# Kernel optimization log

Measured on AMD Instinct MI355X. Metric: run time of the kernel, lower is better.

## Reference

```python
import jax, jax.numpy as jnp
import numpy as np

N_NODES = 20000
N_EDGES = 200000
D_MODEL = 128
N_HEADS = 8
N_LAYERS = 2  # num_gnn - 1 concat layers


def setup_inputs() -> dict:
    key = jax.random.key(0)
    ks = jax.random.split(key, 12)
    s = 0.05  # keep activations well-scaled across residual layers
    hd = D_MODEL // N_HEADS  # 16
    return {
        "x": jax.random.normal(ks[0], (N_NODES, D_MODEL), jnp.float32),
        "src": jax.random.randint(ks[1], (N_EDGES,), 0, N_NODES),
        "dst": jax.random.randint(ks[2], (N_EDGES,), 0, N_NODES),
        "Ws": jax.random.normal(ks[3], (N_LAYERS, D_MODEL, D_MODEL), jnp.float32) * s,
        "als": jax.random.normal(ks[4], (N_LAYERS, N_HEADS, hd), jnp.float32) * s,
        "ars": jax.random.normal(ks[5], (N_LAYERS, N_HEADS, hd), jnp.float32) * s,
        "bs": jax.random.normal(ks[6], (N_LAYERS, D_MODEL), jnp.float32) * s,
        "W_last": jax.random.normal(ks[7], (D_MODEL, N_HEADS * D_MODEL), jnp.float32) * s,
        "al_last": jax.random.normal(ks[8], (N_HEADS, D_MODEL), jnp.float32) * s,
        "ar_last": jax.random.normal(ks[9], (N_HEADS, D_MODEL), jnp.float32) * s,
        "b_last": jax.random.normal(ks[10], (N_HEADS * D_MODEL,), jnp.float32) * s,
    }


def gat_conv(h, src, dst, W, al, ar, b, num_nodes):
    """DGL GATConv (eval mode, dropout off): returns (N, H, D) head outputs."""
    H, D = al.shape
    feat = (h @ W).reshape(num_nodes, H, D)          # (N,H,D)
    el = jnp.sum(feat * al[None], axis=-1)           # (N,H) attn on src side
    er = jnp.sum(feat * ar[None], axis=-1)           # (N,H) attn on dst side
    e = jax.nn.leaky_relu(el[src] + er[dst], 0.2)    # (E,H)
    # edge softmax over incoming edges of each dst node, per head
    m = jax.ops.segment_max(e, dst, num_segments=num_nodes)  # (N,H)
    p = jnp.exp(e - m[dst])                          # (E,H)
    z = jax.ops.segment_sum(p, dst, num_segments=num_nodes)  # (N,H)
    a = p / z[dst]                                   # (E,H)
    msg = feat[src] * a[..., None]                   # (E,H,D) weighted messages
    rst = jax.ops.segment_sum(msg, dst, num_segments=num_nodes)  # (N,H,D)
    return rst + b.reshape(1, H, D)


def reference(x, src, dst, Ws, als, ars, bs, W_last, al_last, ar_last, b_last):
    N = x.shape[0]
    h = x
    for i in range(N_LAYERS):
        temp = gat_conv(h, src, dst, Ws[i], als[i], ars[i], bs[i], N)  # (N,H,hd)
        h = h + jax.nn.elu(temp.reshape(N, -1))       # concat heads, ELU, residual
    temp = gat_conv(h, src, dst, W_last, al_last, ar_last, b_last, N)  # (N,H,D)
    h = h + jnp.mean(temp, axis=1)                    # mean over heads, residual
    return h
```

## Files before the change

kernel.cpp:

```cpp
#include <hip/hip_runtime.h>
#include <math.h>

#define N_NODES 20000
#define N_EDGES 200000
#define DM 128
#define NH 8

typedef __attribute__((ext_vector_type(8))) short bf16x8;
typedef __attribute__((ext_vector_type(4))) float f32x4;

__device__ __forceinline__ unsigned short f2b(float f) {
  unsigned int u = __float_as_uint(f);
  unsigned int r = (u + 0x7FFFu + ((u >> 16) & 1u)) >> 16;
  return (unsigned short)r;
}
__device__ __forceinline__ float b2f(unsigned short s) {
  return __uint_as_float(((unsigned int)s) << 16);
}

__global__ __launch_bounds__(256) void degzero(int* __restrict__ deg) {
  int i = blockIdx.x * 256 + threadIdx.x;
  if (i < N_NODES) deg[i] = 0;
}

__global__ __launch_bounds__(256) void prep_all(
    const float* __restrict__ x, float* __restrict__ h, unsigned short* __restrict__ hb,
    const int* __restrict__ dstE, int* __restrict__ deg, int* __restrict__ rank,
    const float* __restrict__ Ws, unsigned short* __restrict__ wsz,
    const float* __restrict__ W_last, unsigned short* __restrict__ wpsz,
    const float* __restrict__ al_last, const float* __restrict__ ar_last,
    const float* __restrict__ b_last, unsigned short* __restrict__ wlrsz,
    float* __restrict__ mb) {
  int i = blockIdx.x * 256 + threadIdx.x;
  if (i < (N_NODES * DM) / 4) {
    float4 v = ((const float4*)x)[i];
    ((float4*)h)[i] = v;
    ((ushort4*)hb)[i] = make_ushort4(f2b(v.x), f2b(v.y), f2b(v.z), f2b(v.w));
  }
  if (i < N_EDGES) rank[i] = atomicAdd(&deg[dstE[i]], 1);
  if (i < 2 * 16384) {
    int layer = i >> 14;
    int r = i & 16383;
    int j = r & 7, l = (r >> 3) & 63, f = (r >> 9) & 7, ks = r >> 12;
    int k = ks * 32 + ((l >> 4) << 3) + j;
    int n = f * 16 + (l & 15);
    wsz[i] = f2b(Ws[(size_t)layer * 16384 + k * 128 + n]);
  }
  if (i < 131072) {
    int j = i & 7, l = (i >> 3) & 63, f = (i >> 9) & 7, ks = i >> 12;
    int k = ks * 32 + ((l >> 4) << 3) + j;
    int n = f * 16 + (l & 15);
    int h_ = k >> 7, ko = k & 127;
    wpsz[i] = f2b(W_last[(size_t)ko * 1024 + h_ * 128 + n] * 0.125f);
  }
  if (i < 2048) {
    int j = i & 7, l = (i >> 3) & 63, ks = i >> 9;
    int k = ks * 32 + ((l >> 4) << 3) + j;
    int n = l & 15;
    int hh = n & 7;
    const float* av = (n < 8) ? (al_last + hh * 128) : (ar_last + hh * 128);
    float s = 0.f;
    for (int d = 0; d < 128; ++d) s += W_last[(size_t)k * 1024 + hh * 128 + d] * av[d];
    wlrsz[i] = f2b(s);
  }
  if (i < 128) {
    float s = 0.f;
#pragma unroll
    for (int hh = 0; hh < 8; ++hh) s += b_last[hh * 128 + i];
    mb[i] = s * 0.125f;
  }
}

__global__ void scan_deg(const int* __restrict__ deg, int* __restrict__ off) {
  __shared__ int part[1024];
  const int tid = threadIdx.x;
  const int CHUNK = (N_NODES + 1023) / 1024;
  int base = tid * CHUNK;
  int s = 0;
  for (int i = 0; i < CHUNK; ++i) {
    int idx = base + i;
    if (idx < N_NODES) s += deg[idx];
  }
  part[tid] = s;
  __syncthreads();
  for (int ofs = 1; ofs < 1024; ofs <<= 1) {
    int v = (tid >= ofs) ? part[tid - ofs] : 0;
    __syncthreads();
    part[tid] += v;
    __syncthreads();
  }
  int run = (tid > 0) ? part[tid - 1] : 0;
  for (int i = 0; i < CHUNK; ++i) {
    int idx = base + i;
    if (idx < N_NODES) {
      off[idx] = run;
      run += deg[idx];
    }
  }
  if (tid == 0) off[N_NODES] = part[1023];
}

template <int K, bool LAST>
__device__ __forceinline__ void dev_gemm(int tile, const unsigned short* __restrict__ A,
                                         const unsigned short* __restrict__ Bsz,
                                         const float* __restrict__ hres,
                                         const float* __restrict__ mbv,
                                         unsigned short* __restrict__ Cb,
                                         float* __restrict__ Cf,
                                         const float* __restrict__ al,
                                         const float* __restrict__ ar,
                                         float* __restrict__ elr, int lane, int wid) {
  const int wrow = wid & 1, wc = wid >> 1;
  const int r0 = tile * 32;
  const int arow = r0 + wrow * 16 + (lane & 15);
  const int kg = lane >> 4;

  f32x4 acc[4];
#pragma unroll
  for (int fi = 0; fi < 4; ++fi) acc[fi] = {0.f, 0.f, 0.f, 0.f};

  const bf16x8* Ap = (const bf16x8*)(A + (size_t)arow * K + kg * 8);
#pragma unroll 4
  for (int ks = 0; ks < K / 32; ++ks) {
    bf16x8 a = Ap[ks * 4];
#pragma unroll
    for (int fi = 0; fi < 4; ++fi) {
      int f = wc * 4 + fi;
      bf16x8 b = *(const bf16x8*)(Bsz + (((size_t)(ks * 8 + f) * 64 + lane) << 3));
      acc[fi] = __builtin_amdgcn_mfma_f32_16x16x32_bf16(a, b, acc[fi], 0, 0, 0);
    }
  }

  const int rbase = r0 + wrow * 16 + (lane >> 4) * 4;
#pragma unroll
  for (int fi = 0; fi < 4; ++fi) {
    int col = wc * 64 + fi * 16 + (lane & 15);
#pragma unroll
    for (int r = 0; r < 4; ++r) {
      int row = rbase + r;
      float v = acc[fi][r];
      if (LAST)
        Cf[(size_t)row * DM + col] = v + hres[(size_t)row * DM + col] + mbv[col];
      else
        Cb[(size_t)row * DM + col] = f2b(v);
    }
  }

  if (!LAST) {
#pragma unroll
    for (int fi = 0; fi < 4; ++fi) {
      int hh = wc * 4 + fi;
      float alv = al[hh * 16 + (lane & 15)];
      float arv = ar[hh * 16 + (lane & 15)];
#pragma unroll
      for (int r = 0; r < 4; ++r) {
        float pl = acc[fi][r] * alv;
        float pr = acc[fi][r] * arv;
#pragma unroll
        for (int msk = 1; msk < 16; msk <<= 1) {
          pl += __shfl_xor(pl, msk, 64);
          pr += __shfl_xor(pr, msk, 64);
        }
        if ((lane & 15) == 0) {
          int row = rbase + r;
          elr[row * 16 + hh] = pl;
          elr[row * 16 + 8 + hh] = pr;
        }
      }
    }
  }
}

__global__ __launch_bounds__(256) void gemm0_scatter(
    const unsigned short* __restrict__ A, const unsigned short* __restrict__ Bsz,
    unsigned short* __restrict__ Cb, const float* __restrict__ al,
    const float* __restrict__ ar, float* __restrict__ elr, const int* __restrict__ srcE,
    const int* __restrict__ dstE, const int* __restrict__ rank,
    const int* __restrict__ off, int* __restrict__ csr_src) {
  const int bid = blockIdx.x;
  if (bid < N_NODES / 32) {
    dev_gemm<DM, false>(bid, A, Bsz, nullptr, nullptr, Cb, nullptr, al, ar, elr,
                        threadIdx.x & 63, threadIdx.x >> 6);
  } else {
    int e = (bid - N_NODES / 32) * 256 + threadIdx.x;
    if (e < N_EDGES) {
      csr_src[off[dstE[e]] + rank[e]] = srcE[e];
    }
  }
}

template <int K, bool LAST>
__global__ __launch_bounds__(256) void gemm_mfma(
    const unsigned short* __restrict__ A, const unsigned short* __restrict__ Bsz,
    const float* __restrict__ hres, const float* __restrict__ mbv,
    unsigned short* __restrict__ Cb, float* __restrict__ Cf,
    const float* __restrict__ al, const float* __restrict__ ar, float* __restrict__ elr) {
  dev_gemm<K, LAST>(blockIdx.x, A, Bsz, hres, mbv, Cb, Cf, al, ar, elr, threadIdx.x & 63,
                    threadIdx.x >> 6);
}

template <bool ELR>
__global__ __launch_bounds__(256) void fused_small(
    const int* __restrict__ off, const int* __restrict__ csr_src,
    const unsigned short* __restrict__ feat, const float* __restrict__ elr,
    const float* __restrict__ bias, float* __restrict__ h, unsigned short* __restrict__ hb,
    const unsigned short* __restrict__ wlrsz, float* __restrict__ elr_out) {
  __shared__ float a_lds[4][64];
  __shared__ int s_lds[4][8];
  __shared__ float zi_lds[4][8];
  __shared__ __align__(16) unsigned short nh_lds[4][128];
  const int wid = threadIdx.x >> 6;
  const int t = blockIdx.x * 4 + wid;
  const int lane = threadIdx.x & 63;
  const int e_loc = lane >> 3, hh = lane & 7;
  const int hg = lane >> 3;
  const int beg = off[t], end = off[t + 1];
  const float ert = elr[t * 16 + 8 + hh];

  int e = beg + e_loc;
  bool val = e < end;
  int s = val ? csr_src[e] : 0;
  float xl = val ? elr[s * 16 + hh] : 0.f;

  float z = 0.f, acc0 = 0.f, acc1 = 0.f;
  for (int base = beg; base < end; base += 8) {
    float ex = 0.f;
    if (val) {
      float xv = xl + ert;
      xv = xv > 0.f ? xv : 0.2f * xv;
      ex = __expf(xv);
    }
    a_lds[wid][lane] = ex;
    if (hh == 0) s_lds[wid][e_loc] = s;
    __builtin_amdgcn_wave_barrier();
    asm volatile("s_waitcnt lgkmcnt(0)" ::: "memory");
    z += ex;
    int en = base + 8 + e_loc;
    bool valn = en < end;
    int sn = valn ? csr_src[en] : 0;
    float xln = valn ? elr[sn * 16 + hh] : 0.f;
    int n = min(8, end - base);
    for (int e2 = 0; e2 < n; ++e2) {
      int s2 = s_lds[wid][e2];
      float a = a_lds[wid][e2 * 8 + hg];
      unsigned int hv = *(const unsigned int*)&feat[(size_t)s2 * 128 + 2 * lane];
      acc0 += a * b2f((unsigned short)(hv & 0xffffu));
      acc1 += a * b2f((unsigned short)(hv >> 16));
    }
    __builtin_amdgcn_wave_barrier();
    s = sn;
    xl = xln;
    val = valn;
  }
  z += __shfl_xor(z, 8, 64);
  z += __shfl_xor(z, 16, 64);
  z += __shfl_xor(z, 32, 64);
  if (e_loc == 0) zi_lds[wid][hh] = (z > 0.f) ? 1.f / z : 0.f;
  __builtin_amdgcn_wave_barrier();
  asm volatile("s_waitcnt lgkmcnt(0)" ::: "memory");
  float zi = zi_lds[wid][hg];

  float2 bv = *(const float2*)&bias[2 * lane];
  float v0 = acc0 * zi + bv.x;
  float v1 = acc1 * zi + bv.y;
  v0 = v0 > 0.f ? v0 : expm1f(v0);
  v1 = v1 > 0.f ? v1 : expm1f(v1);
  size_t idx = (size_t)t * 128 + 2 * lane;
  float2 hv = *(const float2*)&h[idx];
  float nh0 = hv.x + v0;
  float nh1 = hv.y + v1;
  *(float2*)&h[idx] = make_float2(nh0, nh1);
  unsigned short b0 = f2b(nh0), b1 = f2b(nh1);
  *(ushort2*)&hb[idx] = make_ushort2(b0, b1);

  if (ELR) {
    *(ushort2*)&nh_lds[wid][2 * lane] = make_ushort2(b0, b1);
    __builtin_amdgcn_wave_barrier();
    asm volatile("s_waitcnt lgkmcnt(0)" ::: "memory");
    const int kg = lane >> 4;
    f32x4 acc = {0.f, 0.f, 0.f, 0.f};
#pragma unroll
    for (int ks = 0; ks < 4; ++ks) {
      bf16x8 a = *(const bf16x8*)&nh_lds[wid][ks * 32 + kg * 8];
      bf16x8 b = *(const bf16x8*)(wlrsz + (((size_t)ks * 64 + lane) << 3));
      acc = __builtin_amdgcn_mfma_f32_16x16x32_bf16(a, b, acc, 0, 0, 0);
    }
    if (lane < 16) elr_out[t * 16 + lane] = acc[0];
  }
}

__global__ __launch_bounds__(256) void fused_last(
    const int* __restrict__ off, const int* __restrict__ csr_src,
    const unsigned short* __restrict__ hb, const float* __restrict__ elr,
    unsigned short* __restrict__ g) {
  __shared__ float a_lds[4][64];
  __shared__ int s_lds[4][8];
  __shared__ float zi_lds[4][8];
  const int wid = threadIdx.x >> 6;
  const int t = blockIdx.x * 4 + wid;
  const int lane = threadIdx.x & 63;
  const int e_loc = lane >> 3, hh = lane & 7;
  const int beg = off[t], end = off[t + 1];
  const float ert = elr[t * 16 + 8 + hh];

  int e = beg + e_loc;
  bool val = e < end;
  int s = val ? csr_src[e] : 0;
  float xl = val ? elr[s * 16 + hh] : 0.f;

  float z = 0.f;
  float accA[8], accB[8];
#pragma unroll
  for (int k = 0; k < 8; ++k) accA[k] = accB[k] = 0.f;

  for (int base = beg; base < end; base += 8) {
    float ex = 0.f;
    if (val) {
      float xv = xl + ert;
      xv = xv > 0.f ? xv : 0.2f * xv;
      ex = __expf(xv);
    }
    a_lds[wid][lane] = ex;
    if (hh == 0) s_lds[wid][e_loc] = s;
    __builtin_amdgcn_wave_barrier();
    asm volatile("s_waitcnt lgkmcnt(0)" ::: "memory");
    z += ex;
    int en = base + 8 + e_loc;
    bool valn = en < end;
    int sn = valn ? csr_src[en] : 0;
    float xln = valn ? elr[sn * 16 + hh] : 0.f;
    int n = min(8, end - base);
    for (int e2 = 0; e2 < n; ++e2) {
      int s2 = s_lds[wid][e2];
      float4 pa = *(const float4*)&a_lds[wid][e2 * 8];
      float4 pb = *(const float4*)&a_lds[wid][e2 * 8 + 4];
      unsigned int hv = *(const unsigned int*)&hb[(size_t)s2 * 128 + 2 * lane];
      float h0 = b2f((unsigned short)(hv & 0xffffu));
      float h1 = b2f((unsigned short)(hv >> 16));
      accA[0] += pa.x * h0; accB[0] += pa.x * h1;
      accA[1] += pa.y * h0; accB[1] += pa.y * h1;
      accA[2] += pa.z * h0; accB[2] += pa.z * h1;
      accA[3] += pa.w * h0; accB[3] += pa.w * h1;
      accA[4] += pb.x * h0; accB[4] += pb.x * h1;
      accA[5] += pb.y * h0; accB[5] += pb.y * h1;
      accA[6] += pb.z * h0; accB[6] += pb.z * h1;
      accA[7] += pb.w * h0; accB[7] += pb.w * h1;
    }
    __builtin_amdgcn_wave_barrier();
    s = sn;
    xl = xln;
    val = valn;
  }
  z += __shfl_xor(z, 8, 64);
  z += __shfl_xor(z, 16, 64);
  z += __shfl_xor(z, 32, 64);
  if (e_loc == 0) zi_lds[wid][hh] = (z > 0.f) ? 1.f / z : 0.f;
  __builtin_amdgcn_wave_barrier();
  asm volatile("s_waitcnt lgkmcnt(0)" ::: "memory");
  float4 zia = *(const float4*)&zi_lds[wid][0];
  float4 zib = *(const float4*)&zi_lds[wid][4];
  float ziv[8] = {zia.x, zia.y, zia.z, zia.w, zib.x, zib.y, zib.z, zib.w};
#pragma unroll
  for (int h2 = 0; h2 < 8; ++h2) {
    *(ushort2*)&g[(size_t)t * 1024 + h2 * 128 + 2 * lane] =
        make_ushort2(f2b(accA[h2] * ziv[h2]), f2b(accB[h2] * ziv[h2]));
  }
}

extern "C" void kernel_launch(void* const* d_in, const int* in_sizes, int n_in,
                              void* d_out, int out_size, void* d_ws, size_t ws_size,
                              hipStream_t stream) {
  const float* x = (const float*)d_in[0];
  const int* src = (const int*)d_in[1];
  const int* dst = (const int*)d_in[2];
  const float* Ws = (const float*)d_in[3];
  const float* als = (const float*)d_in[4];
  const float* ars = (const float*)d_in[5];
  const float* bs = (const float*)d_in[6];
  const float* W_last = (const float*)d_in[7];
  const float* al_last = (const float*)d_in[8];
  const float* ar_last = (const float*)d_in[9];
  const float* b_last = (const float*)d_in[10];
  float* out = (float*)d_out;

  float* h = (float*)d_ws;
  float* elr = h + 2560000;
  float* elr2 = elr + 320000;
  float* mb = elr2 + 320000;
  unsigned short* hb = (unsigned short*)(mb + 128);
  unsigned short* feat = hb + 2560000;
  unsigned short* g = feat + 2560000;
  unsigned short* wsz = g + 20480000;
  unsigned short* wpsz = wsz + 32768;
  unsigned short* wlrsz = wpsz + 131072;
  int* deg = (int*)(wlrsz + 2048);
  int* off = deg + N_NODES;
  int* rank = off + N_NODES + 1;
  int* csr_src = rank + N_EDGES;

  const int GB = N_NODES / 32;
  const int FB = N_NODES / 4;
  const int EB = (N_EDGES + 255) / 256;

  degzero<<<(N_NODES + 255) / 256, 256, 0, stream>>>(deg);
  prep_all<<<(N_NODES * DM / 4 + 255) / 256, 256, 0, stream>>>(
      x, h, hb, dst, deg, rank, Ws, wsz, W_last, wpsz, al_last, ar_last, b_last, wlrsz, mb);
  scan_deg<<<1, 1024, 0, stream>>>(deg, off);
  gemm0_scatter<<<GB + EB, 256, 0, stream>>>(hb, wsz, feat, als, ars, elr, src, dst, rank,
                                             off, csr_src);
  fused_small<false><<<FB, 256, 0, stream>>>(off, csr_src, feat, elr, bs, h, hb, nullptr,
                                             nullptr);
  gemm_mfma<DM, false><<<GB, 256, 0, stream>>>(hb, wsz + 16384, nullptr, nullptr, feat,
                                               nullptr, als + 128, ars + 128, elr);
  fused_small<true><<<FB, 256, 0, stream>>>(off, csr_src, feat, elr, bs + 128, h, hb,
                                            wlrsz, elr2);
  fused_last<<<FB, 256, 0, stream>>>(off, csr_src, hb, elr2, g);
  gemm_mfma<NH * DM, true><<<GB, 256, 0, stream>>>(g, wpsz, h, mb, nullptr, out, nullptr,
                                                   nullptr, nullptr);
}
```

Measured before the change: 184.5 us.

## Fuse last-layer aggregation with output projection GEMM through LDS

Merges the last layer's edge aggregation kernel and the final K=1024 projection GEMM into one kernel. Each 1024-thread block aggregates 16 nodes into an LDS tile, then sixteen waves run MFMA over split K halves and reduce through LDS before adding the residual and bias. This removes the 40MB bf16 intermediate g write and read plus one launch. In exchange, per-block occupancy drops with large LDS use and 1024-thread blocks, and each block reloads the projection weights.

```diff
diff --git a/kernel.cpp b/kernel.cpp
--- a/kernel.cpp
+++ b/kernel.cpp
@@ -100,13 +100,10 @@
   if (tid == 0) off[N_NODES] = part[1023];
 }
 
-template <int K, bool LAST>
+template <int K>
 __device__ __forceinline__ void dev_gemm(int tile, const unsigned short* __restrict__ A,
                                          const unsigned short* __restrict__ Bsz,
-                                         const float* __restrict__ hres,
-                                         const float* __restrict__ mbv,
                                          unsigned short* __restrict__ Cb,
-                                         float* __restrict__ Cf,
                                          const float* __restrict__ al,
                                          const float* __restrict__ ar,
                                          float* __restrict__ elr, int lane, int wid) {
@@ -137,35 +134,28 @@
     int col = wc * 64 + fi * 16 + (lane & 15);
 #pragma unroll
     for (int r = 0; r < 4; ++r) {
-      int row = rbase + r;
-      float v = acc[fi][r];
-      if (LAST)
-        Cf[(size_t)row * DM + col] = v + hres[(size_t)row * DM + col] + mbv[col];
-      else
-        Cb[(size_t)row * DM + col] = f2b(v);
-    }
-  }
-
-  if (!LAST) {
-#pragma unroll
-    for (int fi = 0; fi < 4; ++fi) {
-      int hh = wc * 4 + fi;
-      float alv = al[hh * 16 + (lane & 15)];
-      float arv = ar[hh * 16 + (lane & 15)];
-#pragma unroll
-      for (int r = 0; r < 4; ++r) {
-        float pl = acc[fi][r] * alv;
-        float pr = acc[fi][r] * arv;
-#pragma unroll
-        for (int msk = 1; msk < 16; msk <<= 1) {
-          pl += __shfl_xor(pl, msk, 64);
-          pr += __shfl_xor(pr, msk, 64);
-        }
-        if ((lane & 15) == 0) {
-          int row = rbase + r;
-          elr[row * 16 + hh] = pl;
-          elr[row * 16 + 8 + hh] = pr;
-        }
+      Cb[(size_t)(rbase + r) * DM + col] = f2b(acc[fi][r]);
+    }
+  }
+
+#pragma unroll
+  for (int fi = 0; fi < 4; ++fi) {
+    int hh = wc * 4 + fi;
+    float alv = al[hh * 16 + (lane & 15)];
+    float arv = ar[hh * 16 + (lane & 15)];
+#pragma unroll
+    for (int r = 0; r < 4; ++r) {
+      float pl = acc[fi][r] * alv;
+      float pr = acc[fi][r] * arv;
+#pragma unroll
+      for (int msk = 1; msk < 16; msk <<= 1) {
+        pl += __shfl_xor(pl, msk, 64);
+        pr += __shfl_xor(pr, msk, 64);
+      }
+      if ((lane & 15) == 0) {
+        int row = rbase + r;
+        elr[row * 16 + hh] = pl;
+        elr[row * 16 + 8 + hh] = pr;
       }
     }
   }
@@ -179,8 +169,7 @@
     const int* __restrict__ off, int* __restrict__ csr_src) {
   const int bid = blockIdx.x;
   if (bid < N_NODES / 32) {
-    dev_gemm<DM, false>(bid, A, Bsz, nullptr, nullptr, Cb, nullptr, al, ar, elr,
-                        threadIdx.x & 63, threadIdx.x >> 6);
+    dev_gemm<DM>(bid, A, Bsz, Cb, al, ar, elr, threadIdx.x & 63, threadIdx.x >> 6);
   } else {
     int e = (bid - N_NODES / 32) * 256 + threadIdx.x;
     if (e < N_EDGES) {
@@ -189,14 +178,11 @@
   }
 }
 
-template <int K, bool LAST>
 __global__ __launch_bounds__(256) void gemm_mfma(
     const unsigned short* __restrict__ A, const unsigned short* __restrict__ Bsz,
-    const float* __restrict__ hres, const float* __restrict__ mbv,
-    unsigned short* __restrict__ Cb, float* __restrict__ Cf,
-    const float* __restrict__ al, const float* __restrict__ ar, float* __restrict__ elr) {
-  dev_gemm<K, LAST>(blockIdx.x, A, Bsz, hres, mbv, Cb, Cf, al, ar, elr, threadIdx.x & 63,
-                    threadIdx.x >> 6);
+    unsigned short* __restrict__ Cb, const float* __restrict__ al,
+    const float* __restrict__ ar, float* __restrict__ elr) {
+  dev_gemm<DM>(blockIdx.x, A, Bsz, Cb, al, ar, elr, threadIdx.x & 63, threadIdx.x >> 6);
 }
 
 template <bool ELR>
@@ -289,81 +275,118 @@
   }
 }
 
-__global__ __launch_bounds__(256) void fused_last(
+#define GT_STRIDE 1032
+__global__ __launch_bounds__(1024) void agg_gemm16(
     const int* __restrict__ off, const int* __restrict__ csr_src,
     const unsigned short* __restrict__ hb, const float* __restrict__ elr,
-    unsigned short* __restrict__ g) {
-  __shared__ float a_lds[4][64];
-  __shared__ int s_lds[4][8];
-  __shared__ float zi_lds[4][8];
+    const unsigned short* __restrict__ wpsz, const float* __restrict__ hres,
+    const float* __restrict__ mb, float* __restrict__ out) {
+  __shared__ __align__(16) unsigned short gt[16][GT_STRIDE];
+  __shared__ float red[8][64][4];
+  __shared__ float a_lds[16][64];
+  __shared__ int s_lds[16][8];
+  __shared__ float zi_lds[16][8];
   const int wid = threadIdx.x >> 6;
-  const int t = blockIdx.x * 4 + wid;
   const int lane = threadIdx.x & 63;
+  const int t0 = blockIdx.x * 16;
+  const int t = t0 + wid;
   const int e_loc = lane >> 3, hh = lane & 7;
-  const int beg = off[t], end = off[t + 1];
-  const float ert = elr[t * 16 + 8 + hh];
-
-  int e = beg + e_loc;
-  bool val = e < end;
-  int s = val ? csr_src[e] : 0;
-  float xl = val ? elr[s * 16 + hh] : 0.f;
-
-  float z = 0.f;
-  float accA[8], accB[8];
-#pragma unroll
-  for (int k = 0; k < 8; ++k) accA[k] = accB[k] = 0.f;
-
-  for (int base = beg; base < end; base += 8) {
-    float ex = 0.f;
-    if (val) {
-      float xv = xl + ert;
-      xv = xv > 0.f ? xv : 0.2f * xv;
-      ex = __expf(xv);
-    }
-    a_lds[wid][lane] = ex;
-    if (hh == 0) s_lds[wid][e_loc] = s;
+
+  {
+    const int beg = off[t], end = off[t + 1];
+    const float ert = elr[t * 16 + 8 + hh];
+    int e = beg + e_loc;
+    bool val = e < end;
+    int s = val ? csr_src[e] : 0;
+    float xl = val ? elr[s * 16 + hh] : 0.f;
+
+    float z = 0.f;
+    float accA[8], accB[8];
+#pragma unroll
+    for (int k = 0; k < 8; ++k) accA[k] = accB[k] = 0.f;
+
+    for (int base = beg; base < end; base += 8) {
+      float ex = 0.f;
+      if (val) {
+        float xv = xl + ert;
+        xv = xv > 0.f ? xv : 0.2f * xv;
+        ex = __expf(xv);
+      }
+      a_lds[wid][lane] = ex;
+      if (hh == 0) s_lds[wid][e_loc] = s;
+      __builtin_amdgcn_wave_barrier();
+      asm volatile("s_waitcnt lgkmcnt(0)" ::: "memory");
+      z += ex;
+      int en = base + 8 + e_loc;
+      bool valn = en < end;
+      int sn = valn ? csr_src[en] : 0;
+      float xln = valn ? elr[sn * 16 + hh] : 0.f;
+      int n = min(8, end - base);
+      for (int e2 = 0; e2 < n; ++e2) {
+        int s2 = s_lds[wid][e2];
+        float4 pa = *(const float4*)&a_lds[wid][e2 * 8];
+        float4 pb = *(const float4*)&a_lds[wid][e2 * 8 + 4];
+        unsigned int hv = *(const unsigned int*)&hb[(size_t)s2 * 128 + 2 * lane];
+        float h0 = b2f((unsigned short)(hv & 0xffffu));
+        float h1 = b2f((unsigned short)(hv >> 16));
+        accA[0] += pa.x * h0; accB[0] += pa.x * h1;
+        accA[1] += pa.y * h0; accB[1] += pa.y * h1;
+        accA[2] += pa.z * h0; accB[2] += pa.z * h1;
+        accA[3] += pa.w * h0; accB[3] += pa.w * h1;
+        accA[4] += pb.x * h0; accB[4] += pb.x * h1;
+        accA[5] += pb.y * h0; accB[5] += pb.y * h1;
+        accA[6] += pb.z * h0; accB[6] += pb.z * h1;
+        accA[7] += pb.w * h0; accB[7] += pb.w * h1;
+      }
+      __builtin_amdgcn_wave_barrier();
+      s = sn;
+      xl = xln;
+      val = valn;
+    }
+    z += __shfl_xor(z, 8, 64);
+    z += __shfl_xor(z, 16, 64);
+    z += __shfl_xor(z, 32, 64);
+    if (e_loc == 0) zi_lds[wid][hh] = (z > 0.f) ? 1.f / z : 0.f;
     __builtin_amdgcn_wave_barrier();
     asm volatile("s_waitcnt lgkmcnt(0)" ::: "memory");
-    z += ex;
-    int en = base + 8 + e_loc;
-    bool valn = en < end;
-    int sn = valn ? csr_src[en] : 0;
-    float xln = valn ? elr[sn * 16 + hh] : 0.f;
-    int n = min(8, end - base);
-    for (int e2 = 0; e2 < n; ++e2) {
-      int s2 = s_lds[wid][e2];
-      float4 pa = *(const float4*)&a_lds[wid][e2 * 8];
-      float4 pb = *(const float4*)&a_lds[wid][e2 * 8 + 4];
-      unsigned int hv = *(const unsigned int*)&hb[(size_t)s2 * 128 + 2 * lane];
-      float h0 = b2f((unsigned short)(hv & 0xffffu));
-      float h1 = b2f((unsigned short)(hv >> 16));
-      accA[0] += pa.x * h0; accB[0] += pa.x * h1;
-      accA[1] += pa.y * h0; accB[1] += pa.y * h1;
-      accA[2] += pa.z * h0; accB[2] += pa.z * h1;
-      accA[3] += pa.w * h0; accB[3] += pa.w * h1;
-      accA[4] += pb.x * h0; accB[4] += pb.x * h1;
-      accA[5] += pb.y * h0; accB[5] += pb.y * h1;
-      accA[6] += pb.z * h0; accB[6] += pb.z * h1;
-      accA[7] += pb.w * h0; accB[7] += pb.w * h1;
-    }
-    __builtin_amdgcn_wave_barrier();
-    s = sn;
-    xl = xln;
-    val = valn;
-  }
-  z += __shfl_xor(z, 8, 64);
-  z += __shfl_xor(z, 16, 64);
-  z += __shfl_xor(z, 32, 64);
-  if (e_loc == 0) zi_lds[wid][hh] = (z > 0.f) ? 1.f / z : 0.f;
-  __builtin_amdgcn_wave_barrier();
-  asm volatile("s_waitcnt lgkmcnt(0)" ::: "memory");
-  float4 zia = *(const float4*)&zi_lds[wid][0];
-  float4 zib = *(const float4*)&zi_lds[wid][4];
-  float ziv[8] = {zia.x, zia.y, zia.z, zia.w, zib.x, zib.y, zib.z, zib.w};
-#pragma unroll
-  for (int h2 = 0; h2 < 8; ++h2) {
-    *(ushort2*)&g[(size_t)t * 1024 + h2 * 128 + 2 * lane] =
-        make_ushort2(f2b(accA[h2] * ziv[h2]), f2b(accB[h2] * ziv[h2]));
+    float4 zia = *(const float4*)&zi_lds[wid][0];
+    float4 zib = *(const float4*)&zi_lds[wid][4];
+    float ziv[8] = {zia.x, zia.y, zia.z, zia.w, zib.x, zib.y, zib.z, zib.w};
+#pragma unroll
+    for (int h2 = 0; h2 < 8; ++h2) {
+      *(ushort2*)&gt[wid][h2 * 128 + 2 * lane] =
+          make_ushort2(f2b(accA[h2] * ziv[h2]), f2b(accB[h2] * ziv[h2]));
+    }
+  }
+  __syncthreads();
+
+  const int f = wid & 7;
+  const int kh = wid >> 3;
+  const int ar16 = lane & 15;
+  const int kg = lane >> 4;
+  f32x4 acc = {0.f, 0.f, 0.f, 0.f};
+#pragma unroll 4
+  for (int ksl = 0; ksl < 16; ++ksl) {
+    int ks = kh * 16 + ksl;
+    bf16x8 a = *(const bf16x8*)&gt[ar16][ks * 32 + kg * 8];
+    bf16x8 b = *(const bf16x8*)(wpsz + (((size_t)(ks * 8 + f) * 64 + lane) << 3));
+    acc = __builtin_amdgcn_mfma_f32_16x16x32_bf16(a, b, acc, 0, 0, 0);
+  }
+  if (kh == 1) {
+    *(float4*)&red[f][lane][0] = make_float4(acc[0], acc[1], acc[2], acc[3]);
+  }
+  __syncthreads();
+  if (kh == 0) {
+    float4 p = *(const float4*)&red[f][lane][0];
+    const int col = f * 16 + (lane & 15);
+    const int rb = (lane >> 4) * 4;
+    float r4[4] = {p.x, p.y, p.z, p.w};
+#pragma unroll
+    for (int r = 0; r < 4; ++r) {
+      int row = t0 + rb + r;
+      out[(size_t)row * 128 + col] =
+          acc[r] + r4[r] + hres[(size_t)row * 128 + col] + mb[col];
+    }
   }
 }
 
@@ -389,8 +412,7 @@
   float* mb = elr2 + 320000;
   unsigned short* hb = (unsigned short*)(mb + 128);
   unsigned short* feat = hb + 2560000;
-  unsigned short* g = feat + 2560000;
-  unsigned short* wsz = g + 20480000;
+  unsigned short* wsz = feat + 2560000;
   unsigned short* wpsz = wsz + 32768;
   unsigned short* wlrsz = wpsz + 131072;
   int* deg = (int*)(wlrsz + 2048);
@@ -410,11 +432,8 @@
                                              off, csr_src);
   fused_small<false><<<FB, 256, 0, stream>>>(off, csr_src, feat, elr, bs, h, hb, nullptr,
                                              nullptr);
-  gemm_mfma<DM, false><<<GB, 256, 0, stream>>>(hb, wsz + 16384, nullptr, nullptr, feat,
-                                               nullptr, als + 128, ars + 128, elr);
+  gemm_mfma<<<GB, 256, 0, stream>>>(hb, wsz + 16384, feat, als + 128, ars + 128, elr);
   fused_small<true><<<FB, 256, 0, stream>>>(off, csr_src, feat, elr, bs + 128, h, hb,
                                             wlrsz, elr2);
-  fused_last<<<FB, 256, 0, stream>>>(off, csr_src, hb, elr2, g);
-  gemm_mfma<NH * DM, true><<<GB, 256, 0, stream>>>(g, wpsz, h, mb, nullptr, out, nullptr,
-                                                   nullptr, nullptr);
-}
+  agg_gemm16<<<N_NODES / 16, 1024, 0, stream>>>(off, csr_src, hb, elr2, wpsz, h, mb, out);
+}
```

Measured after the change: 176.5 us. -4.4%, faster.
